# Kernel tuning notes

Hardware: AMD Instinct MI355X
Metric: run time of the kernel (lower is better)

## Reference

```python
import jax, jax.numpy as jnp
import numpy as np

B = 16384        # batch
NDIS = 20        # discrete features
NCONT = 10       # continuous features
VOCAB = 100000   # per-feature vocab size
EMB = 32         # embedding_size
E = 8            # expert_num
T = 2            # task_num
H1, H2 = 512, 256  # expert hidden units
DOUT = 128       # expert_out_dim
TH = 64          # task hidden units
DIN = NDIS * EMB + NCONT  # 650 expert input dim
GIN = NDIS + NCONT        # 30 gate input dim


def setup_inputs() -> dict:
    key = jax.random.key(0)
    ks = jax.random.split(key, 20)
    s = 0.02
    return {
        "X_dis": jax.random.randint(ks[0], (B, NDIS), 0, VOCAB, dtype=jnp.int32),
        "X_cont": jax.random.normal(ks[1], (B, NCONT), dtype=jnp.float32),
        # embedding tables (stacked across the NDIS features)
        "lin_emb": jax.random.normal(ks[2], (NDIS, VOCAB, 1), dtype=jnp.float32) * s,
        "deep_emb": jax.random.normal(ks[3], (NDIS, VOCAB, EMB), dtype=jnp.float32) * s,
        # expert MLPs stacked across experts: 650 -> 512 -> 256 -> 128
        "expert_W1": jax.random.normal(ks[4], (E, DIN, H1), dtype=jnp.float32) * s,
        "expert_b1": jnp.zeros((E, H1), dtype=jnp.float32),
        "expert_W2": jax.random.normal(ks[5], (E, H1, H2), dtype=jnp.float32) * s,
        "expert_b2": jnp.zeros((E, H2), dtype=jnp.float32),
        "expert_W3": jax.random.normal(ks[6], (E, H2, DOUT), dtype=jnp.float32) * s,
        "expert_b3": jnp.zeros((E, DOUT), dtype=jnp.float32),
        # per-task gate: Linear(30 -> E)
        "gate_W": jax.random.normal(ks[7], (T, GIN, E), dtype=jnp.float32) * s,
        "gate_b": jnp.zeros((T, E), dtype=jnp.float32),
        # per-task tower: 128 -> 64 -> 1
        "task_W1": jax.random.normal(ks[8], (T, DOUT, TH), dtype=jnp.float32) * s,
        "task_b1": jnp.zeros((T, TH), dtype=jnp.float32),
        "task_W2": jax.random.normal(ks[9], (T, TH, 1), dtype=jnp.float32) * s,
        "task_b2": jnp.zeros((T, 1), dtype=jnp.float32),
    }


def reference(X_dis, X_cont, lin_emb, deep_emb,
              expert_W1, expert_b1, expert_W2, expert_b2, expert_W3, expert_b3,
              gate_W, gate_b, task_W1, task_b1, task_W2, task_b2):
    fidx = jnp.arange(NDIS)[None, :]                      # [1, NDIS]
    # batched embedding gathers across all discrete features
    lin = lin_emb[fidx, X_dis][..., 0]                    # [B, NDIS]
    deep = deep_emb[fidx, X_dis].reshape(X_dis.shape[0], -1)  # [B, NDIS*EMB]
    expert_in = jnp.concatenate([deep, X_cont], axis=1)   # [B, 650]
    gate_in = jnp.concatenate([lin, X_cont], axis=1)      # [B, 30]

    # grouped expert MLPs
    h = jax.nn.relu(jnp.einsum('bi,eih->beh', expert_in, expert_W1) + expert_b1)
    h = jax.nn.relu(jnp.einsum('beh,eho->beo', h, expert_W2) + expert_b2)
    expert_out = jnp.einsum('beh,ehd->bed', h, expert_W3) + expert_b3  # [B, E, DOUT]

    # per-task softmax gates and weighted combine
    gates = jax.nn.softmax(jnp.einsum('bi,tie->bte', gate_in, gate_W) + gate_b, axis=-1)
    task_in = jnp.einsum('bte,bed->btd', gates, expert_out)            # [B, T, DOUT]

    # task towers
    t = jax.nn.relu(jnp.einsum('btd,tdh->bth', task_in, task_W1) + task_b1)
    out = (jnp.einsum('bth,tho->bto', t, task_W2) + task_b2)[..., 0]   # [B, T]
    return out
```

## Files before the change

kernel.cpp:

```cpp
#include <hip/hip_runtime.h>


typedef unsigned short u16;
typedef unsigned int u32;
typedef __attribute__((ext_vector_type(8))) __bf16 bf16x8;
typedef __attribute__((ext_vector_type(4))) float f32x4;
typedef __attribute__((ext_vector_type(4))) unsigned short u16x4;

#define DEVINL __device__ __forceinline__

DEVINL u16 f2bf(float f) {
  union { float f; u32 u; } x; x.f = f;
  u32 u = x.u;
  return (u16)((u + 0x7fffu + ((u >> 16) & 1u)) >> 16);
}
DEVINL float bf2f(u16 h) {
  union { u32 u; float f; } x; x.u = ((u32)h) << 16;
  return x.f;
}
DEVINL void gload16(const u16* g, u16* l) {
  __builtin_amdgcn_global_load_lds((const __attribute__((address_space(1))) void*)g,
                                   (__attribute__((address_space(3))) void*)l,
                                   16, 0, 0);
}

__global__ __launch_bounds__(256)
void transpose_w_kernel(const float* __restrict__ W, u16* __restrict__ WT,
                        int K, int N, int Kpad)
{
  __shared__ float tbuf[16][65];
  const int e = blockIdx.z;
  const float* We = W + (size_t)e * K * N;
  u16* Wt = WT + (size_t)e * N * Kpad;
  const int k0 = blockIdx.x * 16, n0 = blockIdx.y * 64;
#pragma unroll
  for (int p = 0; p < 4; ++p) {
    const int idx = threadIdx.x + p * 256;
    const int nl = idx & 63, kl = idx >> 6;
    const int gk = k0 + kl;
    tbuf[kl][nl] = (gk < K) ? We[(size_t)gk * N + n0 + nl] : 0.f;
  }
  __syncthreads();
#pragma unroll
  for (int p = 0; p < 4; ++p) {
    const int idx = threadIdx.x + p * 256;
    const int kl = idx & 15, nl = idx >> 4;
    Wt[(size_t)(n0 + nl) * Kpad + k0 + kl] = f2bf(tbuf[kl][nl]);
  }
}

__global__ __launch_bounds__(256)
void gather_kernel(const int* __restrict__ Xd, const float* __restrict__ Xc,
                   const float* __restrict__ lin_emb, const float* __restrict__ deep_emb,
                   const float* __restrict__ gW, const float* __restrict__ gb,
                   u16* __restrict__ ein, float* __restrict__ gates,
                   int rowBase, int Bc)
{
  __shared__ float gi[4][32];
  const int wid = threadIdx.x >> 6, lane = threadIdx.x & 63;
  const int rl = blockIdx.x * 4 + wid;
  const int r = rowBase + rl;
  const int* xd = Xd + (size_t)r * 20;
  u16* er = ein + (size_t)rl * 704;
#pragma unroll
  for (int i = 0; i < 3; ++i) {
    const int li = i * 64 + lane;
    if (li < 160) {
      const int f = li >> 3, sub = li & 7;
      const int idx = xd[f];
      const float4 v = *(const float4*)&deep_emb[((size_t)f * 100000 + idx) * 32 + sub * 4];
      u16x4 o;
      o.x = f2bf(v.x); o.y = f2bf(v.y); o.z = f2bf(v.z); o.w = f2bf(v.w);
      *(u16x4*)&er[f * 32 + sub * 4] = o;
    }
  }
  if (lane < 10) er[640 + lane] = f2bf(Xc[(size_t)r * 10 + lane]);
  if (lane < 54) er[650 + lane] = 0;
  if (lane < 20) gi[wid][lane] = lin_emb[(size_t)lane * 100000 + xd[lane]];
  if (lane < 10) gi[wid][20 + lane] = Xc[(size_t)r * 10 + lane];
  asm volatile("s_waitcnt lgkmcnt(0)" ::: "memory");
  float logit = 0.f;
  const int t = lane >> 3, ee = lane & 7;
  if (lane < 16) {
    float a = gb[t * 8 + ee];
#pragma unroll
    for (int i = 0; i < 30; ++i) a += gi[wid][i] * gW[(t * 30 + i) * 8 + ee];
    logit = a;
  }
  float mx = logit;
#pragma unroll
  for (int d = 1; d < 8; d <<= 1) mx = fmaxf(mx, __shfl_xor(mx, d));
  float p = expf(logit - mx);
  float sm = p;
#pragma unroll
  for (int d = 1; d < 8; d <<= 1) sm += __shfl_xor(sm, d);
  if (lane < 16) gates[(size_t)rl * 16 + lane] = p / sm;
}

template<bool RELU, typename CT>
__global__ __launch_bounds__(256, 2)
void gemm_kernel(const u16* __restrict__ A, size_t sAe,
                 const u16* __restrict__ Bw, size_t sBe,
                 CT* __restrict__ C, size_t sCe, int ldc,
                 const float* __restrict__ bias, int N, int K,
                 int nCol, int nRow)
{
  __shared__ u16 As[2][8192];
  __shared__ u16 Bs[2][8192];

  const int perE = nCol * nRow;
  const int work = (blockIdx.x & 7) * perE + (blockIdx.x >> 3);
  const int e  = work / perE;
  const int rem = work - e * perE;
  const int mt = rem / nCol;
  const int ct = rem - mt * nCol;

  const u16* Ae = A + (size_t)e * sAe;
  const u16* Be = Bw + (size_t)e * sBe;
  const int row0 = mt * 128;
  const int col0 = ct * 128;
  const int tid = threadIdx.x;
  const int lane = tid & 63;
  const int wid = tid >> 6;
  const int wr = wid >> 1, wc = wid & 1;

  int rw_[4], gch_[4], ldsOff_[4];
#pragma unroll
  for (int i = 0; i < 4; ++i) {
    const int o = (wid * 4 + i) * 1024 + lane * 16;
    rw_[i] = o >> 7;
    const int ch = (o >> 4) & 7;
    gch_[i] = ch ^ (rw_[i] & 7);
    ldsOff_[i] = (wid * 4 + i) * 512;
  }
  const int KT = K >> 6;

  auto stage = [&](int buf, int kt) {
    const int kb = kt << 6;
#pragma unroll
    for (int i = 0; i < 4; ++i) {
      gload16(Ae + ((size_t)(row0 + rw_[i]) * K + kb + (gch_[i] << 3)),
              &As[buf][ldsOff_[i]]);
      gload16(Be + ((size_t)(col0 + rw_[i]) * K + kb + (gch_[i] << 3)),
              &Bs[buf][ldsOff_[i]]);
    }
  };

  f32x4 acc[4][4];
#pragma unroll
  for (int m = 0; m < 4; ++m)
#pragma unroll
    for (int n = 0; n < 4; ++n) acc[m][n] = {0.f, 0.f, 0.f, 0.f};

  stage(0, 0);
  __syncthreads();

  for (int kt = 0; kt < KT; ++kt) {
    const int cur = kt & 1;
    if (kt + 1 < KT) stage(cur ^ 1, kt + 1);
#pragma unroll
    for (int half = 0; half < 2; ++half) {
      const int kp = half * 4 + (lane >> 4);
      bf16x8 af[4], bfr[4];
#pragma unroll
      for (int m = 0; m < 4; ++m) {
        const int rw = wr * 64 + m * 16 + (lane & 15);
        af[m] = *(const bf16x8*)&As[cur][rw * 64 + ((kp ^ (rw & 7)) << 3)];
      }
#pragma unroll
      for (int n = 0; n < 4; ++n) {
        const int rw = wc * 64 + n * 16 + (lane & 15);
        bfr[n] = *(const bf16x8*)&Bs[cur][rw * 64 + ((kp ^ (rw & 7)) << 3)];
      }
      __builtin_amdgcn_s_setprio(1);
#pragma unroll
      for (int m = 0; m < 4; ++m)
#pragma unroll
        for (int n = 0; n < 4; ++n)
          acc[m][n] = __builtin_amdgcn_mfma_f32_16x16x32_bf16(af[m], bfr[n],
                                                              acc[m][n], 0, 0, 0);
      __builtin_amdgcn_s_setprio(0);
    }
    __syncthreads();
  }

  const int cl = lane & 15;
  const int rl4 = (lane >> 4) * 4;
#pragma unroll
  for (int n = 0; n < 4; ++n) {
    const int col = col0 + wc * 64 + n * 16 + cl;
    const float bv = bias[(size_t)e * N + col];
#pragma unroll
    for (int m = 0; m < 4; ++m) {
      const int grow = row0 + wr * 64 + m * 16 + rl4;
      CT* cp = C + (size_t)e * sCe + (size_t)grow * ldc + col;
#pragma unroll
      for (int j = 0; j < 4; ++j) {
        float v = acc[m][n][j] + bv;
        if (RELU) v = fmaxf(v, 0.f);
        if constexpr (sizeof(CT) == 2) cp[(size_t)j * ldc] = (CT)f2bf(v);
        else                           cp[(size_t)j * ldc] = (CT)v;
      }
    }
  }
}

__global__ __launch_bounds__(256)
void tower_kernel(const u16* __restrict__ eo,
                  const float* __restrict__ gates,
                  const float* __restrict__ tW1,
                  const float* __restrict__ tb1, const float* __restrict__ tW2,
                  const float* __restrict__ tb2, float* __restrict__ out,
                  int rowBase, int Bc)
{
  __shared__ u16 w1s[2 * 128 * 64];
  __shared__ float tin[4][2][128];
  for (int i = threadIdx.x; i < 2 * 128 * 64; i += 256) w1s[i] = f2bf(tW1[i]);
  __syncthreads();
  const int wid = threadIdx.x >> 6, lane = threadIdx.x & 63;
  const int stride = gridDim.x * 4;
  for (int it = 0; it < 4; ++it) {
    const int r = blockIdx.x * 4 + wid + it * stride;
    const float* gp = gates + (size_t)r * 16;
    float g[16];
#pragma unroll
    for (int i = 0; i < 16; ++i) g[i] = gp[i];
    float t0a = 0.f, t0b = 0.f, t1a = 0.f, t1b = 0.f;
#pragma unroll
    for (int ee = 0; ee < 8; ++ee) {
      const u32 pv = *(const u32*)(eo + ((size_t)ee * Bc + r) * 128 + lane * 2);
      const float a = bf2f((u16)(pv & 0xffff));
      const float b = bf2f((u16)(pv >> 16));
      t0a += g[ee] * a;      t0b += g[ee] * b;
      t1a += g[8 + ee] * a;  t1b += g[8 + ee] * b;
    }
    tin[wid][0][lane * 2] = t0a; tin[wid][0][lane * 2 + 1] = t0b;
    tin[wid][1][lane * 2] = t1a; tin[wid][1][lane * 2 + 1] = t1b;
    asm volatile("s_waitcnt lgkmcnt(0)" ::: "memory");
#pragma unroll
    for (int t = 0; t < 2; ++t) {
      float acc = tb1[t * 64 + lane];
#pragma unroll 8
      for (int d = 0; d < 128; ++d)
        acc += tin[wid][t][d] * bf2f(w1s[(t * 128 + d) * 64 + lane]);
      acc = fmaxf(acc, 0.f);
      float s = acc * tW2[t * 64 + lane];
#pragma unroll
      for (int dd = 1; dd < 64; dd <<= 1) s += __shfl_xor(s, dd);
      if (lane == 0) out[(size_t)(rowBase + r) * 2 + t] = s + tb2[t];
    }
    asm volatile("s_waitcnt lgkmcnt(0)" ::: "memory");
  }
}

extern "C" void kernel_launch(void* const* d_in, const int* in_sizes, int n_in,
                              void* d_out, int out_size, void* d_ws, size_t ws_size,
                              hipStream_t stream) {
  const int*   X_dis   = (const int*)  d_in[0];
  const float* X_cont  = (const float*)d_in[1];
  const float* lin_emb = (const float*)d_in[2];
  const float* deep_emb= (const float*)d_in[3];
  const float* eW1     = (const float*)d_in[4];
  const float* eb1     = (const float*)d_in[5];
  const float* eW2     = (const float*)d_in[6];
  const float* eb2     = (const float*)d_in[7];
  const float* eW3     = (const float*)d_in[8];
  const float* eb3     = (const float*)d_in[9];
  const float* gW      = (const float*)d_in[10];
  const float* gb      = (const float*)d_in[11];
  const float* tW1     = (const float*)d_in[12];
  const float* tb1     = (const float*)d_in[13];
  const float* tW2     = (const float*)d_in[14];
  const float* tb2     = (const float*)d_in[15];
  float* out = (float*)d_out;

  char* ws = (char*)d_ws;
  u16* w1t = (u16*)(ws + 0);
  u16* w2t = (u16*)(ws + 5767168);
  u16* w3t = (u16*)(ws + 7864320);
  const size_t base = 8388608;

  const int B = 16384;
  int NC = 1;
  while (NC < 64 && base + (size_t)(B / NC) * 13760ull > ws_size) NC <<= 1;
  const int Bc = B / NC;

  u16*   ein   = (u16*)  (ws + base);
  float* gates = (float*)(ws + base + (size_t)Bc * 1408);
  u16*   h1    = (u16*)  (ws + base + (size_t)Bc * 1472);
  u16*   h2    = (u16*)  (ws + base + (size_t)Bc * 1472 + (size_t)Bc * 8192);
  u16*   eo    = h1;

  transpose_w_kernel<<<dim3(44, 8, 8), 256, 0, stream>>>(eW1, w1t, 650, 512, 704);
  transpose_w_kernel<<<dim3(32, 4, 8), 256, 0, stream>>>(eW2, w2t, 512, 256, 512);
  transpose_w_kernel<<<dim3(16, 2, 8), 256, 0, stream>>>(eW3, w3t, 256, 128, 256);

  for (int c = 0; c < NC; ++c) {
    const int rowBase = c * Bc;
    const int nRow = Bc / 128;
    gather_kernel<<<Bc / 4, 256, 0, stream>>>(X_dis, X_cont, lin_emb, deep_emb,
                                              gW, gb, ein, gates, rowBase, Bc);
    gemm_kernel<true,  u16><<<4 * nRow * 8, 256, 0, stream>>>(
        ein, 0,                 w1t, (size_t)512 * 704,
        h1, (size_t)Bc * 512, 512, eb1, 512, 704, 4, nRow);
    gemm_kernel<true,  u16><<<2 * nRow * 8, 256, 0, stream>>>(
        h1, (size_t)Bc * 512,   w2t, (size_t)256 * 512,
        h2, (size_t)Bc * 256, 256, eb2, 256, 512, 2, nRow);
    gemm_kernel<false, u16><<<1 * nRow * 8, 256, 0, stream>>>(
        h2, (size_t)Bc * 256,   w3t, (size_t)128 * 256,
        eo, (size_t)Bc * 128, 128, eb3, 128, 256, 1, nRow);
    tower_kernel<<<Bc / 16, 256, 0, stream>>>(eo, gates, tW1, tb1, tW2, tb2,
                                              out, rowBase, Bc);
  }
}
```

Measured before the change: 267.4 us.

## Add 256x256-tile 8-wave GEMM with interleaved staging for expert layers 1-2

Adds a new GEMM kernel that runs 512 threads over a 256x256 output tile. It stages A and B into double-buffered LDS and interleaves the next tile's global-to-LDS loads with barrier-separated MFMA phases, using hand-placed waitcnt and sched barriers. The first two expert layers now use it instead of the 128x128 kernel, which raises operand reuse per LDS load and cuts the number of blocks. In exchange it uses much more LDS and registers per block and launches fewer blocks, so per-CU occupancy drops and the tail is coarser.

```diff
diff --git a/kernel.cpp b/kernel.cpp
--- a/kernel.cpp
+++ b/kernel.cpp
@@ -8,6 +8,7 @@
 typedef __attribute__((ext_vector_type(4))) unsigned short u16x4;
 
 #define DEVINL __device__ __forceinline__
+#define MFMA16(a, b, c) __builtin_amdgcn_mfma_f32_16x16x32_bf16(a, b, c, 0, 0, 0)
 
 DEVINL u16 f2bf(float f) {
   union { float f; u32 u; } x; x.f = f;
@@ -97,6 +98,159 @@
   if (lane < 16) gates[(size_t)rl * 16 + lane] = p / sm;
 }
 
+#define AFRAGS(M0, M1)                                                         \
+  a00 = *(const bf16x8*)(As0 + (M0) * 1024 + aoff0);                           \
+  a01 = *(const bf16x8*)(As0 + (M0) * 1024 + aoff1);                           \
+  a10 = *(const bf16x8*)(As0 + (M1) * 1024 + aoff0);                           \
+  a11 = *(const bf16x8*)(As0 + (M1) * 1024 + aoff1);
+
+#define SYNC_MFMA(M0, M1)                                                      \
+  __builtin_amdgcn_s_barrier();                                                \
+  asm volatile("s_waitcnt lgkmcnt(0)" ::: "memory");                           \
+  __builtin_amdgcn_sched_barrier(0);                                           \
+  __builtin_amdgcn_s_setprio(1);                                               \
+  acc[M0][0] = MFMA16(a00, b00, acc[M0][0]);                                   \
+  acc[M0][0] = MFMA16(a01, b01, acc[M0][0]);                                   \
+  acc[M0][1] = MFMA16(a00, b10, acc[M0][1]);                                   \
+  acc[M0][1] = MFMA16(a01, b11, acc[M0][1]);                                   \
+  acc[M0][2] = MFMA16(a00, b20, acc[M0][2]);                                   \
+  acc[M0][2] = MFMA16(a01, b21, acc[M0][2]);                                   \
+  acc[M0][3] = MFMA16(a00, b30, acc[M0][3]);                                   \
+  acc[M0][3] = MFMA16(a01, b31, acc[M0][3]);                                   \
+  acc[M1][0] = MFMA16(a10, b00, acc[M1][0]);                                   \
+  acc[M1][0] = MFMA16(a11, b01, acc[M1][0]);                                   \
+  acc[M1][1] = MFMA16(a10, b10, acc[M1][1]);                                   \
+  acc[M1][1] = MFMA16(a11, b11, acc[M1][1]);                                   \
+  acc[M1][2] = MFMA16(a10, b20, acc[M1][2]);                                   \
+  acc[M1][2] = MFMA16(a11, b21, acc[M1][2]);                                   \
+  acc[M1][3] = MFMA16(a10, b30, acc[M1][3]);                                   \
+  acc[M1][3] = MFMA16(a11, b31, acc[M1][3]);                                   \
+  __builtin_amdgcn_s_setprio(0);                                               \
+  __builtin_amdgcn_s_barrier();
+
+template<bool RELU, typename CT>
+__global__ __launch_bounds__(512, 2)
+void gemm8_kernel(const u16* __restrict__ A, size_t sAe,
+                  const u16* __restrict__ Bw, size_t sBe,
+                  CT* __restrict__ C, size_t sCe, int ldc,
+                  const float* __restrict__ bias, int N, int K,
+                  int nCol, int nRow)
+{
+  __shared__ __align__(16) u16 As[2][2][8192];
+  __shared__ __align__(16) u16 Bs[2][2][8192];
+
+  const int perE = nCol * nRow;
+  const int work = (blockIdx.x & 7) * perE + (blockIdx.x >> 3);
+  const int e = work / perE;
+  const int rem = work - e * perE;
+  const int mt = rem / nCol, ct = rem - mt * nCol;
+
+  const u16* Ae = A + (size_t)e * sAe;
+  const u16* Be = Bw + (size_t)e * sBe;
+  const int row0 = mt * 256, col0 = ct * 256;
+  const int tid = threadIdx.x, lane = tid & 63, wid = tid >> 6;
+  const int wr = wid >> 2, wc = wid & 3;
+  const int KT = K >> 6;
+
+  const int rA = lane >> 3, ch = lane & 7;
+  auto stageA = [&](int buf, int h, int kt) {
+    const int kb = kt << 6;
+#pragma unroll
+    for (int j = 0; j < 2; ++j) {
+      const int s = j * 8 + wid;
+      const int rr = s * 8 + rA;
+      const int gc = ch ^ (rr & 7);
+      gload16(Ae + ((size_t)(row0 + h * 128 + rr) * K + kb + (gc << 3)),
+              &As[buf][h][s * 512]);
+    }
+  };
+  auto stageB = [&](int buf, int h, int kt) {
+    const int kb = kt << 6;
+#pragma unroll
+    for (int j = 0; j < 2; ++j) {
+      const int s = j * 8 + wid;
+      const int rr = s * 8 + rA;
+      const int gc = ch ^ (rr & 7);
+      gload16(Be + ((size_t)(col0 + h * 128 + rr) * K + kb + (gc << 3)),
+              &Bs[buf][h][s * 512]);
+    }
+  };
+
+  const int l15 = lane & 15, l4 = lane >> 4, x0 = lane & 7;
+  const int aoff0 = l15 * 64 + ((l4 ^ x0) << 3);
+  const int aoff1 = l15 * 64 + (((4 + l4) ^ x0) << 3);
+  const int bb = (wc & 1) * 64;
+  const int boff0 = (bb + l15) * 64 + ((l4 ^ x0) << 3);
+  const int boff1 = (bb + l15) * 64 + (((4 + l4) ^ x0) << 3);
+
+  f32x4 acc[8][4];
+#pragma unroll
+  for (int m = 0; m < 8; ++m)
+#pragma unroll
+    for (int n = 0; n < 4; ++n) acc[m][n] = {0.f, 0.f, 0.f, 0.f};
+
+  stageA(0, 0, 0); stageA(0, 1, 0);
+  stageB(0, 0, 0); stageB(0, 1, 0);
+  if (KT > 1) {
+    stageB(1, 0, 1); stageB(1, 1, 1);
+    asm volatile("s_waitcnt vmcnt(4)" ::: "memory");
+  } else {
+    asm volatile("s_waitcnt vmcnt(0)" ::: "memory");
+  }
+  __builtin_amdgcn_s_barrier();
+
+  for (int u = 0; u < KT; ++u) {
+    const int c = u & 1;
+    const u16* As0 = &As[c][wr][0];
+    const u16* Bs0 = &Bs[c][wc >> 1][0];
+    bf16x8 a00, a01, a10, a11;
+    bf16x8 b00 = *(const bf16x8*)(Bs0 + 0 * 1024 + boff0);
+    bf16x8 b01 = *(const bf16x8*)(Bs0 + 0 * 1024 + boff1);
+    bf16x8 b10 = *(const bf16x8*)(Bs0 + 1 * 1024 + boff0);
+    bf16x8 b11 = *(const bf16x8*)(Bs0 + 1 * 1024 + boff1);
+    bf16x8 b20 = *(const bf16x8*)(Bs0 + 2 * 1024 + boff0);
+    bf16x8 b21 = *(const bf16x8*)(Bs0 + 2 * 1024 + boff1);
+    bf16x8 b30 = *(const bf16x8*)(Bs0 + 3 * 1024 + boff0);
+    bf16x8 b31 = *(const bf16x8*)(Bs0 + 3 * 1024 + boff1);
+    AFRAGS(0, 1);
+    if (u + 1 < KT) stageA(c ^ 1, 0, u + 1);
+    SYNC_MFMA(0, 1);
+    AFRAGS(2, 3);
+    if (u + 1 < KT) stageA(c ^ 1, 1, u + 1);
+    SYNC_MFMA(2, 3);
+    AFRAGS(4, 5);
+    if (u + 2 < KT) stageB(c, 0, u + 2);
+    SYNC_MFMA(4, 5);
+    AFRAGS(6, 7);
+    if (u + 2 < KT) {
+      stageB(c, 1, u + 2);
+      asm volatile("s_waitcnt vmcnt(4)" ::: "memory");
+    } else {
+      asm volatile("s_waitcnt vmcnt(0)" ::: "memory");
+    }
+    SYNC_MFMA(6, 7);
+  }
+
+  const int rl4 = l4 * 4;
+#pragma unroll
+  for (int n = 0; n < 4; ++n) {
+    const int col = col0 + wc * 64 + n * 16 + l15;
+    const float bv = bias[(size_t)e * N + col];
+#pragma unroll
+    for (int m = 0; m < 8; ++m) {
+      const int grow = row0 + wr * 128 + m * 16 + rl4;
+      CT* cp = C + (size_t)e * sCe + (size_t)grow * ldc + col;
+#pragma unroll
+      for (int j = 0; j < 4; ++j) {
+        float v = acc[m][n][j] + bv;
+        if (RELU) v = fmaxf(v, 0.f);
+        if constexpr (sizeof(CT) == 2) cp[(size_t)j * ldc] = (CT)f2bf(v);
+        else                           cp[(size_t)j * ldc] = (CT)v;
+      }
+    }
+  }
+}
+
 template<bool RELU, typename CT>
 __global__ __launch_bounds__(256, 2)
 void gemm_kernel(const u16* __restrict__ A, size_t sAe,
@@ -110,7 +264,7 @@
 
   const int perE = nCol * nRow;
   const int work = (blockIdx.x & 7) * perE + (blockIdx.x >> 3);
-  const int e  = work / perE;
+  const int e = work / perE;
   const int rem = work - e * perE;
   const int mt = rem / nCol;
   const int ct = rem - mt * nCol;
@@ -177,8 +331,7 @@
       for (int m = 0; m < 4; ++m)
 #pragma unroll
         for (int n = 0; n < 4; ++n)
-          acc[m][n] = __builtin_amdgcn_mfma_f32_16x16x32_bf16(af[m], bfr[n],
-                                                              acc[m][n], 0, 0, 0);
+          acc[m][n] = MFMA16(af[m], bfr[n], acc[m][n]);
       __builtin_amdgcn_s_setprio(0);
     }
     __syncthreads();
@@ -297,18 +450,18 @@
 
   for (int c = 0; c < NC; ++c) {
     const int rowBase = c * Bc;
-    const int nRow = Bc / 128;
+    const int nRow8 = Bc / 256;
     gather_kernel<<<Bc / 4, 256, 0, stream>>>(X_dis, X_cont, lin_emb, deep_emb,
                                               gW, gb, ein, gates, rowBase, Bc);
-    gemm_kernel<true,  u16><<<4 * nRow * 8, 256, 0, stream>>>(
+    gemm8_kernel<true, u16><<<2 * nRow8 * 8, 512, 0, stream>>>(
         ein, 0,                 w1t, (size_t)512 * 704,
-        h1, (size_t)Bc * 512, 512, eb1, 512, 704, 4, nRow);
-    gemm_kernel<true,  u16><<<2 * nRow * 8, 256, 0, stream>>>(
+        h1, (size_t)Bc * 512, 512, eb1, 512, 704, 2, nRow8);
+    gemm8_kernel<true, u16><<<1 * nRow8 * 8, 512, 0, stream>>>(
         h1, (size_t)Bc * 512,   w2t, (size_t)256 * 512,
-        h2, (size_t)Bc * 256, 256, eb2, 256, 512, 2, nRow);
-    gemm_kernel<false, u16><<<1 * nRow * 8, 256, 0, stream>>>(
+        h2, (size_t)Bc * 256, 256, eb2, 256, 512, 1, nRow8);
+    gemm_kernel<false, u16><<<1 * (Bc / 128) * 8, 256, 0, stream>>>(
         h2, (size_t)Bc * 256,   w3t, (size_t)128 * 256,
-        eo, (size_t)Bc * 128, 128, eb3, 128, 256, 1, nRow);
+        eo, (size_t)Bc * 128, 128, eb3, 128, 256, 1, Bc / 128);
     tower_kernel<<<Bc / 16, 256, 0, stream>>>(eo, gates, tW1, tb1, tW2, tb2,
                                               out, rowBase, Bc);
   }
```

Result: slower. 282.3 us (+5.6%).

## Fuse third expert GEMM with gated expert combine into one kernel

Applied to the files above, without the earlier changes.

Replaces the layer-3 expert GEMM plus the tower kernel's gate-weighted combine with a single kernel. Each block handles 64 rows, loops over all 8 experts, and accumulates the gate-weighted outputs for both tasks in registers. Only the per-task combined inputs are written out in bf16. This avoids writing and re-reading the [E,B,128] expert outputs. In exchange, expert-level parallelism drops: there are fewer blocks, each doing sequential work over experts, and the output tile per block is smaller (64x128).

```diff
diff --git a/kernel.cpp b/kernel.cpp
--- a/kernel.cpp
+++ b/kernel.cpp
@@ -8,6 +8,7 @@
 typedef __attribute__((ext_vector_type(4))) unsigned short u16x4;
 
 #define DEVINL __device__ __forceinline__
+#define MFMA16(a, b, c) __builtin_amdgcn_mfma_f32_16x16x32_bf16(a, b, c, 0, 0, 0)
 
 DEVINL u16 f2bf(float f) {
   union { float f; u32 u; } x; x.f = f;
@@ -177,8 +178,7 @@
       for (int m = 0; m < 4; ++m)
 #pragma unroll
         for (int n = 0; n < 4; ++n)
-          acc[m][n] = __builtin_amdgcn_mfma_f32_16x16x32_bf16(af[m], bfr[n],
-                                                              acc[m][n], 0, 0, 0);
+          acc[m][n] = MFMA16(af[m], bfr[n], acc[m][n]);
       __builtin_amdgcn_s_setprio(0);
     }
     __syncthreads();
@@ -205,44 +205,143 @@
   }
 }
 
+__global__ __launch_bounds__(256, 2)
+void g3c_kernel(const u16* __restrict__ h2, const u16* __restrict__ w3t,
+                const float* __restrict__ eb3, const float* __restrict__ gates,
+                u16* __restrict__ tin, int Bc)
+{
+  __shared__ __align__(16) u16 As[2][4096];
+  __shared__ __align__(16) u16 Bs[2][8192];
+  __shared__ float gl[64 * 16];
+  __shared__ float ebl[8 * 128];
+
+  const int row0 = blockIdx.x * 64;
+  const int tid = threadIdx.x, lane = tid & 63, wv = tid >> 6;
+  const int l15 = lane & 15, l4 = lane >> 4;
+  const int rA = lane >> 3, ch = lane & 7;
+
+  ((float4*)gl)[tid]  = ((const float4*)(gates + (size_t)row0 * 16))[tid];
+  ((float4*)ebl)[tid] = ((const float4*)eb3)[tid];
+
+  auto stageA = [&](int buf, int e, int kt) {
+    const int kb = kt << 6;
+    const u16* h2e = h2 + (size_t)e * Bc * 256;
+#pragma unroll
+    for (int j = 0; j < 2; ++j) {
+      const int s = wv * 2 + j;
+      const int rr = s * 8 + rA;
+      const int gc = ch ^ (rr & 7);
+      gload16(h2e + ((size_t)(row0 + rr) * 256 + kb + (gc << 3)),
+              &As[buf][s * 512]);
+    }
+  };
+  auto stageB = [&](int buf, int e, int kt) {
+    const int kb = kt << 6;
+    const u16* w3e = w3t + (size_t)e * 128 * 256;
+#pragma unroll
+    for (int j = 0; j < 4; ++j) {
+      const int s = wv * 4 + j;
+      const int rr = s * 8 + rA;
+      const int gc = ch ^ (rr & 7);
+      gload16(w3e + ((size_t)rr * 256 + kb + (gc << 3)),
+              &Bs[buf][s * 512]);
+    }
+  };
+
+  f32x4 ti0[8], ti1[8];
+#pragma unroll
+  for (int n = 0; n < 8; ++n) { ti0[n] = {0.f,0.f,0.f,0.f}; ti1[n] = {0.f,0.f,0.f,0.f}; }
+
+  stageA(0, 0, 0); stageB(0, 0, 0);
+  __syncthreads();
+
+  for (int e = 0; e < 8; ++e) {
+    f32x4 acc[8];
+#pragma unroll
+    for (int n = 0; n < 8; ++n) acc[n] = {0.f,0.f,0.f,0.f};
+
+    for (int kt = 0; kt < 4; ++kt) {
+      const int cur = kt & 1;
+      if (kt < 3)          { stageA(cur ^ 1, e, kt + 1);     stageB(cur ^ 1, e, kt + 1); }
+      else if (e + 1 < 8)  { stageA(cur ^ 1, e + 1, 0);      stageB(cur ^ 1, e + 1, 0); }
+#pragma unroll
+      for (int half = 0; half < 2; ++half) {
+        const int kp = half * 4 + l4;
+        const int arow = wv * 16 + l15;
+        const bf16x8 af = *(const bf16x8*)&As[cur][arow * 64 + ((kp ^ (arow & 7)) << 3)];
+        bf16x8 bf[8];
+#pragma unroll
+        for (int n = 0; n < 8; ++n) {
+          const int rb = n * 16 + l15;
+          bf[n] = *(const bf16x8*)&Bs[cur][rb * 64 + ((kp ^ (rb & 7)) << 3)];
+        }
+        __builtin_amdgcn_s_setprio(1);
+#pragma unroll
+        for (int n = 0; n < 8; ++n) acc[n] = MFMA16(af, bf[n], acc[n]);
+        __builtin_amdgcn_s_setprio(0);
+      }
+      __syncthreads();
+    }
+
+    float g0j[4], g1j[4];
+#pragma unroll
+    for (int j = 0; j < 4; ++j) {
+      const int rl = wv * 16 + l4 * 4 + j;
+      g0j[j] = gl[rl * 16 + e];
+      g1j[j] = gl[rl * 16 + 8 + e];
+    }
+#pragma unroll
+    for (int n = 0; n < 8; ++n) {
+      const float bv = ebl[e * 128 + n * 16 + l15];
+#pragma unroll
+      for (int j = 0; j < 4; ++j) {
+        const float v = acc[n][j] + bv;
+        ti0[n][j] += g0j[j] * v;
+        ti1[n][j] += g1j[j] * v;
+      }
+    }
+  }
+
+#pragma unroll
+  for (int n = 0; n < 8; ++n) {
+    const int col = n * 16 + l15;
+#pragma unroll
+    for (int j = 0; j < 4; ++j) {
+      const size_t rg = row0 + wv * 16 + l4 * 4 + j;
+      tin[(rg * 2 + 0) * 128 + col] = f2bf(ti0[n][j]);
+      tin[(rg * 2 + 1) * 128 + col] = f2bf(ti1[n][j]);
+    }
+  }
+}
+
 __global__ __launch_bounds__(256)
-void tower_kernel(const u16* __restrict__ eo,
-                  const float* __restrict__ gates,
+void tower_kernel(const u16* __restrict__ tin,
                   const float* __restrict__ tW1,
                   const float* __restrict__ tb1, const float* __restrict__ tW2,
                   const float* __restrict__ tb2, float* __restrict__ out,
                   int rowBase, int Bc)
 {
   __shared__ u16 w1s[2 * 128 * 64];
-  __shared__ float tin[4][2][128];
+  __shared__ float tinLds[4][2][128];
   for (int i = threadIdx.x; i < 2 * 128 * 64; i += 256) w1s[i] = f2bf(tW1[i]);
   __syncthreads();
   const int wid = threadIdx.x >> 6, lane = threadIdx.x & 63;
   const int stride = gridDim.x * 4;
   for (int it = 0; it < 4; ++it) {
     const int r = blockIdx.x * 4 + wid + it * stride;
-    const float* gp = gates + (size_t)r * 16;
-    float g[16];
-#pragma unroll
-    for (int i = 0; i < 16; ++i) g[i] = gp[i];
-    float t0a = 0.f, t0b = 0.f, t1a = 0.f, t1b = 0.f;
-#pragma unroll
-    for (int ee = 0; ee < 8; ++ee) {
-      const u32 pv = *(const u32*)(eo + ((size_t)ee * Bc + r) * 128 + lane * 2);
-      const float a = bf2f((u16)(pv & 0xffff));
-      const float b = bf2f((u16)(pv >> 16));
-      t0a += g[ee] * a;      t0b += g[ee] * b;
-      t1a += g[8 + ee] * a;  t1b += g[8 + ee] * b;
-    }
-    tin[wid][0][lane * 2] = t0a; tin[wid][0][lane * 2 + 1] = t0b;
-    tin[wid][1][lane * 2] = t1a; tin[wid][1][lane * 2 + 1] = t1b;
+    const u32 p0 = *(const u32*)(tin + ((size_t)r * 2 + 0) * 128 + lane * 2);
+    const u32 p1 = *(const u32*)(tin + ((size_t)r * 2 + 1) * 128 + lane * 2);
+    tinLds[wid][0][lane * 2]     = bf2f((u16)(p0 & 0xffff));
+    tinLds[wid][0][lane * 2 + 1] = bf2f((u16)(p0 >> 16));
+    tinLds[wid][1][lane * 2]     = bf2f((u16)(p1 & 0xffff));
+    tinLds[wid][1][lane * 2 + 1] = bf2f((u16)(p1 >> 16));
     asm volatile("s_waitcnt lgkmcnt(0)" ::: "memory");
 #pragma unroll
     for (int t = 0; t < 2; ++t) {
       float acc = tb1[t * 64 + lane];
 #pragma unroll 8
       for (int d = 0; d < 128; ++d)
-        acc += tin[wid][t][d] * bf2f(w1s[(t * 128 + d) * 64 + lane]);
+        acc += tinLds[wid][t][d] * bf2f(w1s[(t * 128 + d) * 64 + lane]);
       acc = fmaxf(acc, 0.f);
       float s = acc * tW2[t * 64 + lane];
 #pragma unroll
@@ -289,7 +388,7 @@
   float* gates = (float*)(ws + base + (size_t)Bc * 1408);
   u16*   h1    = (u16*)  (ws + base + (size_t)Bc * 1472);
   u16*   h2    = (u16*)  (ws + base + (size_t)Bc * 1472 + (size_t)Bc * 8192);
-  u16*   eo    = h1;
+  u16*   tin   = h1;
 
   transpose_w_kernel<<<dim3(44, 8, 8), 256, 0, stream>>>(eW1, w1t, 650, 512, 704);
   transpose_w_kernel<<<dim3(32, 4, 8), 256, 0, stream>>>(eW2, w2t, 512, 256, 512);
@@ -300,16 +399,14 @@
     const int nRow = Bc / 128;
     gather_kernel<<<Bc / 4, 256, 0, stream>>>(X_dis, X_cont, lin_emb, deep_emb,
                                               gW, gb, ein, gates, rowBase, Bc);
-    gemm_kernel<true,  u16><<<4 * nRow * 8, 256, 0, stream>>>(
+    gemm_kernel<true, u16><<<4 * nRow * 8, 256, 0, stream>>>(
         ein, 0,                 w1t, (size_t)512 * 704,
         h1, (size_t)Bc * 512, 512, eb1, 512, 704, 4, nRow);
-    gemm_kernel<true,  u16><<<2 * nRow * 8, 256, 0, stream>>>(
+    gemm_kernel<true, u16><<<2 * nRow * 8, 256, 0, stream>>>(
         h1, (size_t)Bc * 512,   w2t, (size_t)256 * 512,
         h2, (size_t)Bc * 256, 256, eb2, 256, 512, 2, nRow);
-    gemm_kernel<false, u16><<<1 * nRow * 8, 256, 0, stream>>>(
-        h2, (size_t)Bc * 256,   w3t, (size_t)128 * 256,
-        eo, (size_t)Bc * 128, 128, eb3, 128, 256, 1, nRow);
-    tower_kernel<<<Bc / 16, 256, 0, stream>>>(eo, gates, tW1, tb1, tW2, tb2,
+    g3c_kernel<<<Bc / 64, 256, 0, stream>>>(h2, w3t, eb3, gates, tin, Bc);
+    tower_kernel<<<Bc / 16, 256, 0, stream>>>(tin, tW1, tb1, tW2, tb2,
                                               out, rowBase, Bc);
   }
 }
```

Result: slower. 277.5 us (+3.8%).
